# Performance work log

Hardware: AMD Instinct MI355X
Metric: run time of the kernel (lower is better)

## Reference

```python
import jax, jax.numpy as jnp
import numpy as np

N = 2048      # nodes per graph
Q = 9         # output_dim (emotion nodes)
D = 256       # input_dim == hidden_dim
L = 4         # num_layers - 1 GIN layers
B = 32        # batch
E = 32768     # edges per graph
EPS = 1e-5    # BatchNorm eps


def _bn(x, g, b, m, v):
    # eval-mode BatchNorm1d over last (channel) dim
    return (x - m) * (g * jax.lax.rsqrt(v + EPS)) + b


def setup_inputs() -> dict:
    key = jax.random.key(0)
    ks = jax.random.split(key, 18)
    s = 1.0 / np.sqrt(D)
    return {
        "batch_feature": jax.random.normal(ks[0], (B, N, D), jnp.float32),
        "edge_mat": jax.random.randint(ks[1], (2, E), 0, N, dtype=jnp.int32),
        "emotion_emb": jax.random.normal(ks[2], (1, Q, D), jnp.float32) * 0.05,
        "mlp_w1": jax.random.normal(ks[3], (L, D, D), jnp.float32) * s,
        "mlp_b1": jnp.zeros((L, D), jnp.float32),
        "mlp_bn_g": jnp.ones((L, D), jnp.float32),
        "mlp_bn_b": jnp.zeros((L, D), jnp.float32),
        "mlp_bn_m": jax.random.normal(ks[4], (L, D), jnp.float32) * 0.1,
        "mlp_bn_v": jax.random.uniform(ks[5], (L, D), jnp.float32, 0.5, 1.5),
        "mlp_w2": jax.random.normal(ks[6], (L, D, D), jnp.float32) * s,
        "mlp_b2": jnp.zeros((L, D), jnp.float32),
        "bn_g": jnp.ones((L, D), jnp.float32),
        "bn_b": jnp.zeros((L, D), jnp.float32),
        "bn_m": jax.random.normal(ks[7], (L, D), jnp.float32) * 0.1,
        "bn_v": jax.random.uniform(ks[8], (L, D), jnp.float32, 0.5, 1.5),
        "pred_w": jax.random.normal(ks[9], (L + 1, D), jnp.float32) * s,
        "pred_b": jnp.zeros((L + 1,), jnp.float32),
    }


def reference(batch_feature, edge_mat, emotion_emb, mlp_w1, mlp_b1,
              mlp_bn_g, mlp_bn_b, mlp_bn_m, mlp_bn_v, mlp_w2, mlp_b2,
              bn_g, bn_b, bn_m, bn_v, pred_w, pred_b):
    # overwrite first Q node rows with shared emotion embeddings
    h = batch_feature.at[:, :Q, :].set(emotion_emb)          # [B, N, D]
    src, dst = edge_mat[0], edge_mat[1]

    def spmm(x):
        # Adj @ x with self-loops; graph topology shared across batch.
        gathered = x[:, dst, :]                              # [B, E, D]
        agg = jax.vmap(
            lambda g: jax.ops.segment_sum(g, src, num_segments=N)
        )(gathered)                                          # [B, N, D]
        return agg + x  # self-loop (identity added to adjacency)

    hidden = [h]
    for l in range(L):
        pooled = spmm(h)
        # 2-layer GIN MLP: Linear -> BN -> ReLU -> Linear
        t = jnp.einsum('bnd,de->bne', pooled, mlp_w1[l]) + mlp_b1[l]
        t = jax.nn.relu(_bn(t, mlp_bn_g[l], mlp_bn_b[l], mlp_bn_m[l], mlp_bn_v[l]))
        t = jnp.einsum('bnd,de->bne', t, mlp_w2[l]) + mlp_b2[l]
        # outer BatchNorm + ReLU
        h = jax.nn.relu(_bn(t, bn_g[l], bn_b[l], bn_m[l], bn_v[l]))
        hidden.append(h)

    score = jnp.zeros((B, Q), jnp.float32)
    for l, hl in enumerate(hidden):
        h_emotion = hl[:, :Q, :]                             # [B, Q, D]
        score = score + jnp.einsum('bqd,d->bq', h_emotion, pred_w[l]) + pred_b[l]
    return jax.nn.sigmoid(score)                             # [B, Q]
```

## Files before the change

### kernel.cpp

```cpp
#include <hip/hip_runtime.h>
#include <hip/hip_bf16.h>

#define NN 2048
#define QQ 9
#define DD 256
#define LL 4
#define BB 32
#define EE 32768
#define EPSV 1e-5f

typedef __attribute__((ext_vector_type(8))) short bf16x8;
typedef __attribute__((ext_vector_type(8))) ushort u16x8;
typedef __attribute__((ext_vector_type(4))) float f32x4;
typedef __attribute__((ext_vector_type(4))) int i32x4;

__device__ __forceinline__ ushort f2bf(float x)
{
    uint u = __float_as_uint(x);
    u += 0x7FFFu + ((u >> 16) & 1u);
    return (ushort)(u >> 16);
}
__device__ __forceinline__ float bf2f(ushort h)
{
    return __uint_as_float(((uint)h) << 16);
}

__global__ void k_count(const int* __restrict__ src, int* __restrict__ cnt)
{
    int e = blockIdx.x * blockDim.x + threadIdx.x;
    if (e < EE) atomicAdd(&cnt[src[e]], 1);
}

__global__ __launch_bounds__(256) void k_scan(const int* __restrict__ cnt,
                                              int* __restrict__ row_ptr,
                                              int* __restrict__ cursor)
{
    __shared__ int part[256];
    int t = threadIdx.x;
    int local[8];
    int s = 0;
    #pragma unroll
    for (int i = 0; i < 8; ++i) { local[i] = cnt[t * 8 + i]; s += local[i]; }
    part[t] = s;
    __syncthreads();
    for (int off = 1; off < 256; off <<= 1) {
        int v = (t >= off) ? part[t - off] : 0;
        __syncthreads();
        part[t] += v;
        __syncthreads();
    }
    int run = part[t] - s;
    #pragma unroll
    for (int i = 0; i < 8; ++i) {
        int idx = t * 8 + i;
        row_ptr[idx] = run;
        cursor[idx]  = run;
        run += local[i];
    }
    if (t == 255) row_ptr[NN] = run;
}

__global__ void k_fill(const int* __restrict__ src, const int* __restrict__ dst,
                       int* __restrict__ cursor, int* __restrict__ col)
{
    int e = blockIdx.x * blockDim.x + threadIdx.x;
    if (e < EE) {
        int p = atomicAdd(&cursor[src[e]], 1);
        col[p] = dst[e];
    }
}

__global__ void k_prep0(const float4* __restrict__ bf, const float4* __restrict__ emo,
                        ushort4* __restrict__ hhi)
{
    int total = BB * NN * (DD / 4);
    for (int idx = blockIdx.x * blockDim.x + threadIdx.x; idx < total;
         idx += gridDim.x * blockDim.x) {
        int d4 = idx & 63;
        int n  = (idx >> 6) & (NN - 1);
        float4 v = (n < QQ) ? emo[n * 64 + d4] : bf[idx];
        ushort4 h;
        h.x = f2bf(v.x); h.y = f2bf(v.y); h.z = f2bf(v.z); h.w = f2bf(v.w);
        hhi[idx] = h;
    }
}

__global__ __launch_bounds__(256) void k_spmm6(
    const ushort* __restrict__ phi,
    const int* __restrict__ row_ptr, const int* __restrict__ col,
    ushort* __restrict__ ohi)
{
    int x     = blockIdx.x & 7;
    int local = blockIdx.x >> 3;
    int w     = threadIdx.x >> 6;
    int t     = threadIdx.x & 63;
    int inst  = local * 4 + w;
    int pl    = inst >> 11;
    int n     = inst & (NN - 1);
    int b     = x * 4 + pl * 2 + (t >> 5);
    int q     = t & 31;
    const ushort* base = phi + (size_t)b * NN * DD + q * 8;

    u16x8 sv = *(const u16x8*)(base + (size_t)n * DD);
    float a[8];
    #pragma unroll
    for (int k = 0; k < 8; ++k) a[k] = bf2f((ushort)sv[k]);

    int beg = row_ptr[n], end = row_ptr[n + 1];
    int j = beg;
    for (; j < end && (j & 3); ++j) {
        u16x8 g = *(const u16x8*)(base + (size_t)col[j] * DD);
        #pragma unroll
        for (int k = 0; k < 8; ++k) a[k] += bf2f((ushort)g[k]);
    }
    for (; j + 8 <= end; j += 8) {
        i32x4 c0 = *(const i32x4*)(col + j);
        i32x4 c1 = *(const i32x4*)(col + j + 4);
        u16x8 g[8];
        g[0] = *(const u16x8*)(base + (size_t)c0.x * DD);
        g[1] = *(const u16x8*)(base + (size_t)c0.y * DD);
        g[2] = *(const u16x8*)(base + (size_t)c0.z * DD);
        g[3] = *(const u16x8*)(base + (size_t)c0.w * DD);
        g[4] = *(const u16x8*)(base + (size_t)c1.x * DD);
        g[5] = *(const u16x8*)(base + (size_t)c1.y * DD);
        g[6] = *(const u16x8*)(base + (size_t)c1.z * DD);
        g[7] = *(const u16x8*)(base + (size_t)c1.w * DD);
        #pragma unroll
        for (int u = 0; u < 8; ++u)
            #pragma unroll
            for (int k = 0; k < 8; ++k) a[k] += bf2f((ushort)g[u][k]);
    }
    if (j + 4 <= end) {
        i32x4 c = *(const i32x4*)(col + j);
        u16x8 g[4];
        g[0] = *(const u16x8*)(base + (size_t)c.x * DD);
        g[1] = *(const u16x8*)(base + (size_t)c.y * DD);
        g[2] = *(const u16x8*)(base + (size_t)c.z * DD);
        g[3] = *(const u16x8*)(base + (size_t)c.w * DD);
        #pragma unroll
        for (int u = 0; u < 4; ++u)
            #pragma unroll
            for (int k = 0; k < 8; ++k) a[k] += bf2f((ushort)g[u][k]);
        j += 4;
    }
    for (; j < end; ++j) {
        u16x8 g = *(const u16x8*)(base + (size_t)col[j] * DD);
        #pragma unroll
        for (int k = 0; k < 8; ++k) a[k] += bf2f((ushort)g[k]);
    }

    u16x8 o;
    #pragma unroll
    for (int k = 0; k < 8; ++k) o[k] = f2bf(a[k]);
    *(u16x8*)(ohi + ((size_t)b * NN + n) * DD + q * 8) = o;
}

__global__ __launch_bounds__(256) void k_wprep(const float* __restrict__ w1,
                                               const float* __restrict__ w2,
                                               ushort* __restrict__ wt_hi)
{
    __shared__ float tile[32][36];
    int bx = blockIdx.x;
    int mat = bx >> 6;
    int tt  = bx & 63;
    int tk = (tt >> 3) * 32;
    int tn = (tt & 7) * 32;
    const float* src = (mat < 4) ? (w1 + (size_t)mat * DD * DD)
                                 : (w2 + (size_t)(mat - 4) * DD * DD);
    int t = threadIdx.x;
    int r = t >> 3, c0 = (t & 7) * 4;
    float4 v = *(const float4*)(src + (size_t)(tk + r) * DD + tn + c0);
    tile[r][c0 + 0] = v.x; tile[r][c0 + 1] = v.y;
    tile[r][c0 + 2] = v.z; tile[r][c0 + 3] = v.w;
    __syncthreads();
    int nn = t >> 3, kq = (t & 7) * 4;
    ushort4 hh;
    hh.x = f2bf(tile[kq + 0][nn]); hh.y = f2bf(tile[kq + 1][nn]);
    hh.z = f2bf(tile[kq + 2][nn]); hh.w = f2bf(tile[kq + 3][nn]);
    size_t off = (size_t)mat * DD * DD + (size_t)(tn + nn) * DD + tk + kq;
    *(ushort4*)(wt_hi + off) = hh;
}

__global__ __launch_bounds__(256, 2) void k_gemm_fused(
    const ushort* __restrict__ A, const ushort* __restrict__ W1t,
    const ushort* __restrict__ W2t,
    const float* __restrict__ b1, const float* __restrict__ g1,
    const float* __restrict__ be1, const float* __restrict__ m1,
    const float* __restrict__ v1,
    const float* __restrict__ b2, const float* __restrict__ g2,
    const float* __restrict__ be2, const float* __restrict__ m2,
    const float* __restrict__ v2,
    ushort* __restrict__ O)
{
    __shared__ alignas(16) ushort As[64][40];
    __shared__ alignas(16) ushort Ws[256][40];
    __shared__ alignas(16) ushort Ts[64][264];

    int tid = threadIdx.x;
    int x  = blockIdx.x & 7;
    int lm = blockIdx.x >> 3;
    int m0 = x * 8192 + lm * 64;
    int lane = tid & 63;
    int w = tid >> 6;
    int wm = w & 1, wn = w >> 1;
    int lr = lane & 15, kg = lane >> 4;
    int rg = lane >> 4;

    f32x4 acc[2][8];
    #pragma unroll
    for (int m = 0; m < 2; ++m)
        #pragma unroll
        for (int n = 0; n < 8; ++n) acc[m][n] = (f32x4)0.f;

    for (int kc = 0; kc < 8; ++kc) {
        int k0 = kc * 32;
        __syncthreads();
        {
            int r = tid >> 2, k8 = (tid & 3) * 8;
            *(float4*)&As[r][k8] = *(const float4*)(A + (size_t)(m0 + r) * DD + k0 + k8);
        }
        #pragma unroll
        for (int i = 0; i < 4; ++i) {
            int idx = tid + i * 256;
            int r = idx >> 2, k8 = (idx & 3) * 8;
            *(float4*)&Ws[r][k8] = *(const float4*)(W1t + (size_t)r * DD + k0 + k8);
        }
        __syncthreads();
        bf16x8 ah[2], bh[8];
        #pragma unroll
        for (int m = 0; m < 2; ++m)
            ah[m] = *(const bf16x8*)&As[wm * 32 + m * 16 + lr][kg * 8];
        #pragma unroll
        for (int n = 0; n < 8; ++n)
            bh[n] = *(const bf16x8*)&Ws[wn * 128 + n * 16 + lr][kg * 8];
        #pragma unroll
        for (int m = 0; m < 2; ++m)
            #pragma unroll
            for (int n = 0; n < 8; ++n)
                acc[m][n] = __builtin_amdgcn_mfma_f32_16x16x32_bf16(ah[m], bh[n], acc[m][n], 0, 0, 0);
    }
    {
        float sN[8], svN[8];
        #pragma unroll
        for (int n = 0; n < 8; ++n) {
            int jj = wn * 128 + n * 16 + lr;
            sN[n]  = g1[jj] * rsqrtf(v1[jj] + EPSV);
            svN[n] = (b1[jj] - m1[jj]) * sN[n] + be1[jj];
        }
        #pragma unroll
        for (int m = 0; m < 2; ++m)
            #pragma unroll
            for (int n = 0; n < 8; ++n) {
                int cc = wn * 128 + n * 16 + lr;
                #pragma unroll
                for (int r = 0; r < 4; ++r) {
                    float y = acc[m][n][r] * sN[n] + svN[n];
                    Ts[wm * 32 + m * 16 + rg * 4 + r][cc] = f2bf(y > 0.f ? y : 0.f);
                }
            }
    }
    #pragma unroll
    for (int m = 0; m < 2; ++m)
        #pragma unroll
        for (int n = 0; n < 8; ++n) acc[m][n] = (f32x4)0.f;

    for (int kc = 0; kc < 8; ++kc) {
        int k0 = kc * 32;
        __syncthreads();
        #pragma unroll
        for (int i = 0; i < 4; ++i) {
            int idx = tid + i * 256;
            int r = idx >> 2, k8 = (idx & 3) * 8;
            *(float4*)&Ws[r][k8] = *(const float4*)(W2t + (size_t)r * DD + k0 + k8);
        }
        __syncthreads();
        bf16x8 ah[2], bh[8];
        #pragma unroll
        for (int m = 0; m < 2; ++m)
            ah[m] = *(const bf16x8*)&Ts[wm * 32 + m * 16 + lr][k0 + kg * 8];
        #pragma unroll
        for (int n = 0; n < 8; ++n)
            bh[n] = *(const bf16x8*)&Ws[wn * 128 + n * 16 + lr][kg * 8];
        #pragma unroll
        for (int m = 0; m < 2; ++m)
            #pragma unroll
            for (int n = 0; n < 8; ++n)
                acc[m][n] = __builtin_amdgcn_mfma_f32_16x16x32_bf16(ah[m], bh[n], acc[m][n], 0, 0, 0);
    }
    __syncthreads();

    {
        float sN[8], svN[8];
        #pragma unroll
        for (int n = 0; n < 8; ++n) {
            int jj = wn * 128 + n * 16 + lr;
            sN[n]  = g2[jj] * rsqrtf(v2[jj] + EPSV);
            svN[n] = (b2[jj] - m2[jj]) * sN[n] + be2[jj];
        }
        #pragma unroll
        for (int m = 0; m < 2; ++m)
            #pragma unroll
            for (int n = 0; n < 8; ++n) {
                int cc = wn * 128 + n * 16 + lr;
                #pragma unroll
                for (int r = 0; r < 4; ++r) {
                    float y = acc[m][n][r] * sN[n] + svN[n];
                    Ts[wm * 32 + m * 16 + rg * 4 + r][cc] = f2bf(y > 0.f ? y : 0.f);
                }
            }
        #pragma unroll
        for (int i = 0; i < 8; ++i) {
            int cid = lane + i * 64;
            int row = cid >> 4, c8 = cid & 15;
            u16x8 vv = *(const u16x8*)&Ts[wm * 32 + row][wn * 128 + c8 * 8];
            *(u16x8*)(O + (size_t)(m0 + wm * 32 + row) * DD + wn * 128 + c8 * 8) = vv;
        }
    }
}

__global__ __launch_bounds__(64) void k_score0(const float4* __restrict__ emo,
                                               const float4* __restrict__ pw,
                                               const float* __restrict__ pb,
                                               float* __restrict__ out)
{
    int q = blockIdx.x, t = threadIdx.x;
    float4 e = emo[q * 64 + t], wv = pw[t];
    float s = e.x * wv.x + e.y * wv.y + e.z * wv.z + e.w * wv.w;
    #pragma unroll
    for (int off = 32; off > 0; off >>= 1) s += __shfl_down(s, off);
    if (t == 0) {
        s += pb[0];
        for (int b = 0; b < BB; ++b) out[b * QQ + q] = s;
    }
}

__global__ __launch_bounds__(64) void k_score2(const ushort4* __restrict__ hhi,
                                               const float4* __restrict__ pw,
                                               const float* __restrict__ pb, int l,
                                               float* __restrict__ out)
{
    int bid = blockIdx.x;
    int b = bid / QQ, q = bid % QQ;
    int t = threadIdx.x;
    size_t o = ((size_t)b * NN + q) * 64 + t;
    ushort4 hh = hhi[o];
    float4 wv = pw[l * 64 + t];
    float sum = bf2f(hh.x) * wv.x + bf2f(hh.y) * wv.y +
                bf2f(hh.z) * wv.z + bf2f(hh.w) * wv.w;
    #pragma unroll
    for (int off = 32; off > 0; off >>= 1) sum += __shfl_down(sum, off);
    if (t == 0) out[bid] += sum + pb[l];
}

__global__ void k_sigmoid(float* out)
{
    int i = threadIdx.x + blockIdx.x * blockDim.x;
    if (i < BB * QQ) out[i] = 1.f / (1.f + expf(-out[i]));
}

extern "C" void kernel_launch(void* const* d_in, const int* in_sizes, int n_in,
                              void* d_out, int out_size, void* d_ws, size_t ws_size,
                              hipStream_t stream)
{
    const float* batch = (const float*)d_in[0];
    const int*   edges = (const int*)d_in[1];
    const float* emo   = (const float*)d_in[2];
    const float* w1    = (const float*)d_in[3];
    const float* b1    = (const float*)d_in[4];
    const float* m_g   = (const float*)d_in[5];
    const float* m_b   = (const float*)d_in[6];
    const float* m_m   = (const float*)d_in[7];
    const float* m_v   = (const float*)d_in[8];
    const float* w2    = (const float*)d_in[9];
    const float* b2    = (const float*)d_in[10];
    const float* g_g   = (const float*)d_in[11];
    const float* g_b   = (const float*)d_in[12];
    const float* g_m   = (const float*)d_in[13];
    const float* g_v   = (const float*)d_in[14];
    const float* pw    = (const float*)d_in[15];
    const float* pb    = (const float*)d_in[16];
    float* out = (float*)d_out;

    const size_t HSZ = (size_t)BB * NN * DD;
    const size_t WT  = (size_t)8 * DD * DD;

    ushort* h_hi = (ushort*)d_ws;
    ushort* P_hi = h_hi + HSZ;
    ushort* wt_hi = P_hi + HSZ;
    int* cnt     = (int*)(wt_hi + WT);
    int* row_ptr = cnt + NN;
    int* cursor  = row_ptr + (NN + 4);
    int* col     = cursor + NN;

    const int* src = edges;
    const int* dst = edges + EE;

    hipMemsetAsync(cnt, 0, NN * sizeof(int), stream);
    k_count<<<EE / 256, 256, 0, stream>>>(src, cnt);
    k_scan<<<1, 256, 0, stream>>>(cnt, row_ptr, cursor);
    k_fill<<<EE / 256, 256, 0, stream>>>(src, dst, cursor, col);
    k_wprep<<<512, 256, 0, stream>>>(w1, w2, wt_hi);
    k_prep0<<<4096, 256, 0, stream>>>((const float4*)batch, (const float4*)emo,
                                      (ushort4*)h_hi);
    k_score0<<<QQ, 64, 0, stream>>>((const float4*)emo, (const float4*)pw, pb, out);

    for (int l = 0; l < LL; ++l) {
        k_spmm6<<<8192, 256, 0, stream>>>(h_hi, row_ptr, col, P_hi);
        k_gemm_fused<<<1024, 256, 0, stream>>>(
            P_hi,
            wt_hi + (size_t)l * DD * DD, wt_hi + (size_t)(4 + l) * DD * DD,
            b1 + l * DD, m_g + l * DD, m_b + l * DD, m_m + l * DD, m_v + l * DD,
            b2 + l * DD, g_g + l * DD, g_b + l * DD, g_m + l * DD, g_v + l * DD,
            h_hi);
        k_score2<<<BB * QQ, 64, 0, stream>>>((const ushort4*)h_hi,
                                             (const float4*)pw, pb, l + 1, out);
    }
    k_sigmoid<<<1, 288, 0, stream>>>(out);
}
```

Before: 334.5 us.

## Split fused GEMM across 8 waves and pack LDS epilogue writes via lane shuffles

Doubles the block to 512 threads so each of 8 waves computes a 32x64 output tile instead of 32x128, halving per-thread accumulators and raising occupancy. Weight tile loads are redistributed across the larger block. The epilogue now exchanges bf16 values between neighbouring lanes with shuffles so it writes 32-bit words to shared memory instead of 16-bit scalars, reducing LDS store count. In exchange, each block reloads the shared weights with more waves contending for the same barriers, and there are extra shuffle instructions.

```diff
diff --git a/kernel.cpp b/kernel.cpp
--- a/kernel.cpp
+++ b/kernel.cpp
@@ -181,7 +181,7 @@
     *(ushort4*)(wt_hi + off) = hh;
 }
 
-__global__ __launch_bounds__(256, 2) void k_gemm_fused(
+__global__ __launch_bounds__(512, 4) void k_gemm_fused(
     const ushort* __restrict__ A, const ushort* __restrict__ W1t,
     const ushort* __restrict__ W2t,
     const float* __restrict__ b1, const float* __restrict__ g1,
@@ -206,114 +206,140 @@
     int lr = lane & 15, kg = lane >> 4;
     int rg = lane >> 4;
 
-    f32x4 acc[2][8];
+    f32x4 acc[2][4];
     #pragma unroll
     for (int m = 0; m < 2; ++m)
         #pragma unroll
-        for (int n = 0; n < 8; ++n) acc[m][n] = (f32x4)0.f;
+        for (int n = 0; n < 4; ++n) acc[m][n] = (f32x4)0.f;
 
     for (int kc = 0; kc < 8; ++kc) {
         int k0 = kc * 32;
         __syncthreads();
-        {
+        if (tid < 256) {
             int r = tid >> 2, k8 = (tid & 3) * 8;
             *(float4*)&As[r][k8] = *(const float4*)(A + (size_t)(m0 + r) * DD + k0 + k8);
         }
         #pragma unroll
-        for (int i = 0; i < 4; ++i) {
-            int idx = tid + i * 256;
+        for (int i = 0; i < 2; ++i) {
+            int idx = tid + i * 512;
             int r = idx >> 2, k8 = (idx & 3) * 8;
             *(float4*)&Ws[r][k8] = *(const float4*)(W1t + (size_t)r * DD + k0 + k8);
         }
         __syncthreads();
-        bf16x8 ah[2], bh[8];
+        bf16x8 ah[2], bh[4];
         #pragma unroll
         for (int m = 0; m < 2; ++m)
             ah[m] = *(const bf16x8*)&As[wm * 32 + m * 16 + lr][kg * 8];
         #pragma unroll
-        for (int n = 0; n < 8; ++n)
-            bh[n] = *(const bf16x8*)&Ws[wn * 128 + n * 16 + lr][kg * 8];
-        #pragma unroll
-        for (int m = 0; m < 2; ++m)
-            #pragma unroll
-            for (int n = 0; n < 8; ++n)
+        for (int n = 0; n < 4; ++n)
+            bh[n] = *(const bf16x8*)&Ws[wn * 64 + n * 16 + lr][kg * 8];
+        #pragma unroll
+        for (int m = 0; m < 2; ++m)
+            #pragma unroll
+            for (int n = 0; n < 4; ++n)
                 acc[m][n] = __builtin_amdgcn_mfma_f32_16x16x32_bf16(ah[m], bh[n], acc[m][n], 0, 0, 0);
     }
     {
-        float sN[8], svN[8];
-        #pragma unroll
-        for (int n = 0; n < 8; ++n) {
-            int jj = wn * 128 + n * 16 + lr;
+        float sN[4], svN[4];
+        #pragma unroll
+        for (int n = 0; n < 4; ++n) {
+            int jj = wn * 64 + n * 16 + lr;
             sN[n]  = g1[jj] * rsqrtf(v1[jj] + EPSV);
             svN[n] = (b1[jj] - m1[jj]) * sN[n] + be1[jj];
         }
         #pragma unroll
         for (int m = 0; m < 2; ++m)
             #pragma unroll
-            for (int n = 0; n < 8; ++n) {
-                int cc = wn * 128 + n * 16 + lr;
+            for (int n = 0; n < 4; ++n) {
+                int cc = wn * 64 + n * 16 + lr;
+                ushort h[4];
                 #pragma unroll
                 for (int r = 0; r < 4; ++r) {
                     float y = acc[m][n][r] * sN[n] + svN[n];
-                    Ts[wm * 32 + m * 16 + rg * 4 + r][cc] = f2bf(y > 0.f ? y : 0.f);
+                    h[r] = f2bf(y > 0.f ? y : 0.f);
+                }
+                uint own01 = (uint)h[0] | ((uint)h[1] << 16);
+                uint own23 = (uint)h[2] | ((uint)h[3] << 16);
+                uint p01 = (uint)__shfl_xor((int)own01, 1);
+                uint p23 = (uint)__shfl_xor((int)own23, 1);
+                int row0 = wm * 32 + m * 16 + rg * 4;
+                if ((lr & 1) == 0) {
+                    *(uint*)&Ts[row0 + 0][cc] = (own01 & 0xffffu) | (p01 << 16);
+                    *(uint*)&Ts[row0 + 1][cc] = (own01 >> 16) | (p01 & 0xffff0000u);
+                } else {
+                    *(uint*)&Ts[row0 + 2][cc - 1] = (p23 & 0xffffu) | (own23 << 16);
+                    *(uint*)&Ts[row0 + 3][cc - 1] = (p23 >> 16) | (own23 & 0xffff0000u);
                 }
             }
     }
     #pragma unroll
     for (int m = 0; m < 2; ++m)
         #pragma unroll
-        for (int n = 0; n < 8; ++n) acc[m][n] = (f32x4)0.f;
+        for (int n = 0; n < 4; ++n) acc[m][n] = (f32x4)0.f;
 
     for (int kc = 0; kc < 8; ++kc) {
         int k0 = kc * 32;
         __syncthreads();
         #pragma unroll
-        for (int i = 0; i < 4; ++i) {
-            int idx = tid + i * 256;
+        for (int i = 0; i < 2; ++i) {
+            int idx = tid + i * 512;
             int r = idx >> 2, k8 = (idx & 3) * 8;
             *(float4*)&Ws[r][k8] = *(const float4*)(W2t + (size_t)r * DD + k0 + k8);
         }
         __syncthreads();
-        bf16x8 ah[2], bh[8];
+        bf16x8 ah[2], bh[4];
         #pragma unroll
         for (int m = 0; m < 2; ++m)
             ah[m] = *(const bf16x8*)&Ts[wm * 32 + m * 16 + lr][k0 + kg * 8];
         #pragma unroll
-        for (int n = 0; n < 8; ++n)
-            bh[n] = *(const bf16x8*)&Ws[wn * 128 + n * 16 + lr][kg * 8];
-        #pragma unroll
-        for (int m = 0; m < 2; ++m)
-            #pragma unroll
-            for (int n = 0; n < 8; ++n)
+        for (int n = 0; n < 4; ++n)
+            bh[n] = *(const bf16x8*)&Ws[wn * 64 + n * 16 + lr][kg * 8];
+        #pragma unroll
+        for (int m = 0; m < 2; ++m)
+            #pragma unroll
+            for (int n = 0; n < 4; ++n)
                 acc[m][n] = __builtin_amdgcn_mfma_f32_16x16x32_bf16(ah[m], bh[n], acc[m][n], 0, 0, 0);
     }
     __syncthreads();
 
     {
-        float sN[8], svN[8];
-        #pragma unroll
-        for (int n = 0; n < 8; ++n) {
-            int jj = wn * 128 + n * 16 + lr;
+        float sN[4], svN[4];
+        #pragma unroll
+        for (int n = 0; n < 4; ++n) {
+            int jj = wn * 64 + n * 16 + lr;
             sN[n]  = g2[jj] * rsqrtf(v2[jj] + EPSV);
             svN[n] = (b2[jj] - m2[jj]) * sN[n] + be2[jj];
         }
         #pragma unroll
         for (int m = 0; m < 2; ++m)
             #pragma unroll
-            for (int n = 0; n < 8; ++n) {
-                int cc = wn * 128 + n * 16 + lr;
+            for (int n = 0; n < 4; ++n) {
+                int cc = wn * 64 + n * 16 + lr;
+                ushort h[4];
                 #pragma unroll
                 for (int r = 0; r < 4; ++r) {
                     float y = acc[m][n][r] * sN[n] + svN[n];
-                    Ts[wm * 32 + m * 16 + rg * 4 + r][cc] = f2bf(y > 0.f ? y : 0.f);
+                    h[r] = f2bf(y > 0.f ? y : 0.f);
+                }
+                uint own01 = (uint)h[0] | ((uint)h[1] << 16);
+                uint own23 = (uint)h[2] | ((uint)h[3] << 16);
+                uint p01 = (uint)__shfl_xor((int)own01, 1);
+                uint p23 = (uint)__shfl_xor((int)own23, 1);
+                int row0 = wm * 32 + m * 16 + rg * 4;
+                if ((lr & 1) == 0) {
+                    *(uint*)&Ts[row0 + 0][cc] = (own01 & 0xffffu) | (p01 << 16);
+                    *(uint*)&Ts[row0 + 1][cc] = (own01 >> 16) | (p01 & 0xffff0000u);
+                } else {
+                    *(uint*)&Ts[row0 + 2][cc - 1] = (p23 & 0xffffu) | (own23 << 16);
+                    *(uint*)&Ts[row0 + 3][cc - 1] = (p23 >> 16) | (own23 & 0xffff0000u);
                 }
             }
         #pragma unroll
-        for (int i = 0; i < 8; ++i) {
+        for (int i = 0; i < 4; ++i) {
             int cid = lane + i * 64;
-            int row = cid >> 4, c8 = cid & 15;
-            u16x8 vv = *(const u16x8*)&Ts[wm * 32 + row][wn * 128 + c8 * 8];
-            *(u16x8*)(O + (size_t)(m0 + wm * 32 + row) * DD + wn * 128 + c8 * 8) = vv;
+            int row = cid >> 3, c8 = cid & 7;
+            u16x8 vv = *(const u16x8*)&Ts[wm * 32 + row][wn * 64 + c8 * 8];
+            *(u16x8*)(O + (size_t)(m0 + wm * 32 + row) * DD + wn * 64 + c8 * 8) = vv;
         }
     }
 }
@@ -406,7 +432,7 @@
 
     for (int l = 0; l < LL; ++l) {
         k_spmm6<<<8192, 256, 0, stream>>>(h_hi, row_ptr, col, P_hi);
-        k_gemm_fused<<<1024, 256, 0, stream>>>(
+        k_gemm_fused<<<1024, 512, 0, stream>>>(
             P_hi,
             wt_hi + (size_t)l * DD * DD, wt_hi + (size_t)(4 + l) * DD * DD,
             b1 + l * DD, m_g + l * DD, m_b + l * DD, m_m + l * DD, m_v + l * DD,
```

Measured after the change: 343.3 us. 2.6% more time.

## Double-buffer GEMM tiles via register prefetch and fuse score/sigmoid into epilogue

Applied to the files above, without the earlier changes.

The fused GIN MLP kernel now prefetches the next K-slice of activations and weights into registers while computing on a double-buffered LDS tile. This halves the barriers per K step and hides global load latency. The per-layer score kernel and the final sigmoid are folded into the GEMM epilogue of the block that owns each graph's first rows, which removes extra launches. It raises LDS use, and the unpadded 32-element row stride may cause bank conflicts on fragment reads.

```diff
diff --git a/kernel.cpp b/kernel.cpp
--- a/kernel.cpp
+++ b/kernel.cpp
@@ -190,10 +190,11 @@
     const float* __restrict__ b2, const float* __restrict__ g2,
     const float* __restrict__ be2, const float* __restrict__ m2,
     const float* __restrict__ v2,
-    ushort* __restrict__ O)
-{
-    __shared__ alignas(16) ushort As[64][40];
-    __shared__ alignas(16) ushort Ws[256][40];
+    const float* __restrict__ pw, const float* __restrict__ pb, int l,
+    ushort* __restrict__ O, float* __restrict__ out)
+{
+    __shared__ alignas(16) ushort As[2][64 * 32];
+    __shared__ alignas(16) ushort Ws[2][256 * 32];
     __shared__ alignas(16) ushort Ts[64][264];
 
     int tid = threadIdx.x;
@@ -206,38 +207,57 @@
     int lr = lane & 15, kg = lane >> 4;
     int rg = lane >> 4;
 
+    int ar = tid >> 2, ak = (tid & 3) * 8;
+    const ushort* Ab = A + (size_t)(m0 + ar) * DD + ak;
+
     f32x4 acc[2][8];
     #pragma unroll
     for (int m = 0; m < 2; ++m)
         #pragma unroll
         for (int n = 0; n < 8; ++n) acc[m][n] = (f32x4)0.f;
 
+    float4 rA;
+    float4 rW[4];
+    rA = *(const float4*)(Ab);
+    #pragma unroll
+    for (int i = 0; i < 4; ++i) {
+        int idx = tid + i * 256;
+        int r = idx >> 2, k8 = (idx & 3) * 8;
+        rW[i] = *(const float4*)(W1t + (size_t)r * DD + k8);
+    }
+    int cur = 0;
     for (int kc = 0; kc < 8; ++kc) {
-        int k0 = kc * 32;
-        __syncthreads();
-        {
-            int r = tid >> 2, k8 = (tid & 3) * 8;
-            *(float4*)&As[r][k8] = *(const float4*)(A + (size_t)(m0 + r) * DD + k0 + k8);
-        }
+        *(float4*)&As[cur][ar * 32 + ak] = rA;
         #pragma unroll
         for (int i = 0; i < 4; ++i) {
             int idx = tid + i * 256;
             int r = idx >> 2, k8 = (idx & 3) * 8;
-            *(float4*)&Ws[r][k8] = *(const float4*)(W1t + (size_t)r * DD + k0 + k8);
+            *(float4*)&Ws[cur][r * 32 + k8] = rW[i];
         }
         __syncthreads();
+        if (kc < 7) {
+            int k0n = (kc + 1) * 32;
+            rA = *(const float4*)(Ab + k0n);
+            #pragma unroll
+            for (int i = 0; i < 4; ++i) {
+                int idx = tid + i * 256;
+                int r = idx >> 2, k8 = (idx & 3) * 8;
+                rW[i] = *(const float4*)(W1t + (size_t)r * DD + k0n + k8);
+            }
+        }
         bf16x8 ah[2], bh[8];
         #pragma unroll
         for (int m = 0; m < 2; ++m)
-            ah[m] = *(const bf16x8*)&As[wm * 32 + m * 16 + lr][kg * 8];
+            ah[m] = *(const bf16x8*)&As[cur][(wm * 32 + m * 16 + lr) * 32 + kg * 8];
         #pragma unroll
         for (int n = 0; n < 8; ++n)
-            bh[n] = *(const bf16x8*)&Ws[wn * 128 + n * 16 + lr][kg * 8];
+            bh[n] = *(const bf16x8*)&Ws[cur][(wn * 128 + n * 16 + lr) * 32 + kg * 8];
         #pragma unroll
         for (int m = 0; m < 2; ++m)
             #pragma unroll
             for (int n = 0; n < 8; ++n)
                 acc[m][n] = __builtin_amdgcn_mfma_f32_16x16x32_bf16(ah[m], bh[n], acc[m][n], 0, 0, 0);
+        cur ^= 1;
     }
     {
         float sN[8], svN[8];
@@ -264,28 +284,45 @@
         #pragma unroll
         for (int n = 0; n < 8; ++n) acc[m][n] = (f32x4)0.f;
 
+    __syncthreads();
+
+    #pragma unroll
+    for (int i = 0; i < 4; ++i) {
+        int idx = tid + i * 256;
+        int r = idx >> 2, k8 = (idx & 3) * 8;
+        rW[i] = *(const float4*)(W2t + (size_t)r * DD + k8);
+    }
+    cur = 0;
     for (int kc = 0; kc < 8; ++kc) {
-        int k0 = kc * 32;
-        __syncthreads();
         #pragma unroll
         for (int i = 0; i < 4; ++i) {
             int idx = tid + i * 256;
             int r = idx >> 2, k8 = (idx & 3) * 8;
-            *(float4*)&Ws[r][k8] = *(const float4*)(W2t + (size_t)r * DD + k0 + k8);
+            *(float4*)&Ws[cur][r * 32 + k8] = rW[i];
         }
         __syncthreads();
+        if (kc < 7) {
+            int k0n = (kc + 1) * 32;
+            #pragma unroll
+            for (int i = 0; i < 4; ++i) {
+                int idx = tid + i * 256;
+                int r = idx >> 2, k8 = (idx & 3) * 8;
+                rW[i] = *(const float4*)(W2t + (size_t)r * DD + k0n + k8);
+            }
+        }
         bf16x8 ah[2], bh[8];
         #pragma unroll
         for (int m = 0; m < 2; ++m)
-            ah[m] = *(const bf16x8*)&Ts[wm * 32 + m * 16 + lr][k0 + kg * 8];
+            ah[m] = *(const bf16x8*)&Ts[wm * 32 + m * 16 + lr][kc * 32 + kg * 8];
         #pragma unroll
         for (int n = 0; n < 8; ++n)
-            bh[n] = *(const bf16x8*)&Ws[wn * 128 + n * 16 + lr][kg * 8];
+            bh[n] = *(const bf16x8*)&Ws[cur][(wn * 128 + n * 16 + lr) * 32 + kg * 8];
         #pragma unroll
         for (int m = 0; m < 2; ++m)
             #pragma unroll
             for (int n = 0; n < 8; ++n)
                 acc[m][n] = __builtin_amdgcn_mfma_f32_16x16x32_bf16(ah[m], bh[n], acc[m][n], 0, 0, 0);
+        cur ^= 1;
     }
     __syncthreads();
 
@@ -316,6 +353,23 @@
             *(u16x8*)(O + (size_t)(m0 + wm * 32 + row) * DD + wn * 128 + c8 * 8) = vv;
         }
     }
+
+    __syncthreads();
+    if ((m0 & (NN - 1)) == 0) {
+        int b = m0 >> 11;
+        for (int q = w; q < QQ; q += 4) {
+            ushort4 hv = *(const ushort4*)&Ts[q][lane * 4];
+            const float4 wv = *(const float4*)&pw[(l + 1) * DD + lane * 4];
+            float s = bf2f(hv.x) * wv.x + bf2f(hv.y) * wv.y +
+                      bf2f(hv.z) * wv.z + bf2f(hv.w) * wv.w;
+            #pragma unroll
+            for (int off = 32; off > 0; off >>= 1) s += __shfl_down(s, off);
+            if (lane == 0) {
+                float v = out[b * QQ + q] + s + pb[l + 1];
+                out[b * QQ + q] = (l == LL - 1) ? 1.f / (1.f + expf(-v)) : v;
+            }
+        }
+    }
 }
 
 __global__ __launch_bounds__(64) void k_score0(const float4* __restrict__ emo,
@@ -332,30 +386,6 @@
         s += pb[0];
         for (int b = 0; b < BB; ++b) out[b * QQ + q] = s;
     }
-}
-
-__global__ __launch_bounds__(64) void k_score2(const ushort4* __restrict__ hhi,
-                                               const float4* __restrict__ pw,
-                                               const float* __restrict__ pb, int l,
-                                               float* __restrict__ out)
-{
-    int bid = blockIdx.x;
-    int b = bid / QQ, q = bid % QQ;
-    int t = threadIdx.x;
-    size_t o = ((size_t)b * NN + q) * 64 + t;
-    ushort4 hh = hhi[o];
-    float4 wv = pw[l * 64 + t];
-    float sum = bf2f(hh.x) * wv.x + bf2f(hh.y) * wv.y +
-                bf2f(hh.z) * wv.z + bf2f(hh.w) * wv.w;
-    #pragma unroll
-    for (int off = 32; off > 0; off >>= 1) sum += __shfl_down(sum, off);
-    if (t == 0) out[bid] += sum + pb[l];
-}
-
-__global__ void k_sigmoid(float* out)
-{
-    int i = threadIdx.x + blockIdx.x * blockDim.x;
-    if (i < BB * QQ) out[i] = 1.f / (1.f + expf(-out[i]));
 }
 
 extern "C" void kernel_launch(void* const* d_in, const int* in_sizes, int n_in,
@@ -411,9 +441,7 @@
             wt_hi + (size_t)l * DD * DD, wt_hi + (size_t)(4 + l) * DD * DD,
             b1 + l * DD, m_g + l * DD, m_b + l * DD, m_m + l * DD, m_v + l * DD,
             b2 + l * DD, g_g + l * DD, g_b + l * DD, g_m + l * DD, g_v + l * DD,
-            h_hi);
-        k_score2<<<BB * QQ, 64, 0, stream>>>((const ushort4*)h_hi,
-                                             (const float4*)pw, pb, l + 1, out);
-    }
-    k_sigmoid<<<1, 288, 0, stream>>>(out);
-}
+            pw, pb, l,
+            h_hi, out);
+    }
+}
```

New measurement: 316.7 us. 1.06x faster.
